# Kernel tuning notes

Measured on AMD Instinct MI355X. Metric: run time of the kernel, lower is better.

The kernel has to match this reference:

```python
import jax, jax.numpy as jnp
import numpy as np

B, T, E, H = 64, 577, 768, 64
GRID_H, GRID_W = 24, 24
NUM_PREFIX = 1
N = GRID_H * GRID_W  # 576 patches
EPS = 1e-5


def setup_inputs() -> dict:
    key = jax.random.key(0)
    ks = jax.random.split(key, 12)
    s = lambda k, shape, fan: jax.random.normal(k, shape, jnp.float32) / np.sqrt(fan)
    return {
        "x": jax.random.normal(ks[0], (B, T, E), jnp.float32),
        "w_q": s(ks[1], (E, H), E),
        "w_k": s(ks[2], (E, H), E),
        "w_v": s(ks[3], (E, H), E),
        "q_gamma": jnp.ones((H,), jnp.float32),
        "q_beta": jnp.zeros((H,), jnp.float32),
        "k_gamma": jnp.ones((H,), jnp.float32),
        "k_beta": jnp.zeros((H,), jnp.float32),
        "w_sigma": s(ks[4], (H, 2), H),
        "b_sigma": jnp.zeros((2,), jnp.float32),
        "w_alpha": s(ks[5], (H, 1), H),
        "b_alpha": jnp.zeros((1,), jnp.float32),
    }


def _layernorm(x, gamma, beta):
    mu = jnp.mean(x, axis=-1, keepdims=True)
    var = jnp.mean(jnp.square(x - mu), axis=-1, keepdims=True)
    return (x - mu) * jax.lax.rsqrt(var + EPS) * gamma + beta


def _grid_sq_dists():
    # coords[i] = (row, col) of patch i; squared coordinate differences [N, N]
    coords = jnp.stack(
        jnp.meshgrid(jnp.arange(GRID_H), jnp.arange(GRID_W), indexing="ij"), axis=-1
    ).reshape(N, 2).astype(jnp.float32)
    diff = coords[:, None, :] - coords[None, :, :]  # [N, N, 2]
    dy2 = jnp.square(diff[..., 0])  # row diff squared
    dx2 = jnp.square(diff[..., 1])  # col diff squared
    return dx2, dy2


def reference(x, w_q, w_k, w_v, q_gamma, q_beta, k_gamma, k_beta,
              w_sigma, b_sigma, w_alpha, b_alpha):
    q = _layernorm(x @ w_q, q_gamma, q_beta)  # [B, T, H]
    k = _layernorm(x @ w_k, k_gamma, k_beta)  # [B, T, H]
    v = x @ w_v                               # [B, T, H]

    sim = jnp.einsum("bqh,bkh->bqk", q, k)    # [B, T, T]

    q_nc = q[:, NUM_PREFIX:, :]               # [B, N, H]
    alpha = jax.nn.softplus(q_nc @ w_alpha + b_alpha)[..., 0]  # [B, N]
    sigma = jax.nn.sigmoid(q_nc @ w_sigma + b_sigma)           # [B, N, 2]
    sx = sigma[..., 0]  # [B, N]
    sy = sigma[..., 1]

    dx2, dy2 = _grid_sq_dists()  # [N, N] each
    # Gaussian decay bias: query-patch p controls sigma; [B, N, N]
    G = jnp.exp(
        -dx2[None] / (2.0 * jnp.square(sx)[:, :, None])
        - dy2[None] / (2.0 * jnp.square(sy)[:, :, None])
    )
    S = alpha[:, :, None] * G

    sim = sim.at[:, NUM_PREFIX:, NUM_PREFIX:].add(S)

    scale = jnp.sqrt(jnp.float32(H))
    attn = jax.nn.softmax(sim / scale, axis=-1)
    return attn @ v  # [B, T, H]
```

## Files before the change

kernel.cpp:

```cpp
#include <hip/hip_runtime.h>
#include <math.h>

#define B_ 64
#define T_ 577
#define E_ 768
#define H_ 64
#define N_ 576
#define GW_ 24

typedef float f32x4 __attribute__((ext_vector_type(4)));
typedef __bf16 bf16x8 __attribute__((ext_vector_type(8)));
typedef __bf16 bf16x4 __attribute__((ext_vector_type(4)));

__device__ inline void split_bf16(float f, __bf16& h, __bf16& l) {
  h = (__bf16)f;
  l = (__bf16)(f - (float)h);
}

__device__ inline float bperm_f(int byte_addr, float x) {
  return __int_as_float(__builtin_amdgcn_ds_bpermute(byte_addr, __float_as_int(x)));
}

#define GLOAD_LDS16(G, L)                                                     \
  __builtin_amdgcn_global_load_lds(                                           \
      (const __attribute__((address_space(1))) void*)(G),                     \
      (__attribute__((address_space(3))) void*)(L), 16, 0, 0)

__global__ __launch_bounds__(256) void prep_w_kernel(
    const float* __restrict__ wq, const float* __restrict__ wk, const float* __restrict__ wv,
    __bf16* __restrict__ wsw2)
{
  int t = blockIdx.x * 256 + threadIdx.x;
  if (t >= 24*192) return;
  int kc = t / 192, n = t - kc*192;
  const float* src = (n < 64) ? wq : ((n < 128) ? wk : wv);
  int nn = n & 63;
  int xb = (n & 3) ^ ((n >> 2) & 3);
  size_t cbase = (size_t)kc * 12288;
  #pragma unroll
  for (int g = 0; g < 4; ++g) {
    __bf16 hb[8], lb[8];
    #pragma unroll
    for (int j = 0; j < 8; ++j) {
      float f = src[(size_t)(kc*32 + g*8 + j)*64 + nn];
      split_bf16(f, hb[j], lb[j]);
    }
    int slot = n*4 + (g ^ xb);
    *(bf16x8*)(wsw2 + cbase + slot*8)        = *(bf16x8*)hb;
    *(bf16x8*)(wsw2 + cbase + 6144 + slot*8) = *(bf16x8*)lb;
  }
}

__global__ __launch_bounds__(256) void qkv_ln_kernel(
    const float* __restrict__ x, const __bf16* __restrict__ wsw2,
    const float* __restrict__ qg, const float* __restrict__ qb,
    const float* __restrict__ kg, const float* __restrict__ kb,
    const float* __restrict__ wsig, const float* __restrict__ bsig,
    const float* __restrict__ walp, const float* __restrict__ balp,
    float* __restrict__ qo, float* __restrict__ ko, float* __restrict__ vo,
    float* __restrict__ alo, float* __restrict__ sxo, float* __restrict__ syo)
{
  __shared__ __align__(16) float smem[64*193 + 256];
  __bf16* A_hi = (__bf16*)smem;
  __bf16* A_lo = A_hi + 2560;
  __bf16* B0   = A_lo + 2560;
  float (*Cs)[193] = (float (*)[193])smem;
  float* mu_q = smem + 64*193;
  float* rs_q = mu_q + 64;
  float* mu_k = rs_q + 64;
  float* rs_k = mu_k + 64;

  const int tid  = threadIdx.x;
  const int lane = tid & 63;
  const int w    = tid >> 6;
  const int quad = lane >> 4;
  const int m    = lane & 15;
  const int rowbase = blockIdx.x << 6;

  f32x4 acc[4][3];
  #pragma unroll
  for (int mt = 0; mt < 4; ++mt)
    #pragma unroll
    for (int nt = 0; nt < 3; ++nt)
      acc[mt][nt] = (f32x4){0.f, 0.f, 0.f, 0.f};

  const int kfrag = quad * 8;
  const int xl    = quad ^ (m & 3) ^ (m >> 2);

  float4 xr0, xr1;
  const int arow0 = tid >> 3,         ak0 = (tid & 7) * 4;
  const int arow1 = (tid + 256) >> 3, ak1 = (tid & 7) * 4;

  auto load_A = [&](int kc) {
    xr0 = *(const float4*)(x + (size_t)(rowbase + arow0)*E_ + kc*32 + ak0);
    xr1 = *(const float4*)(x + (size_t)(rowbase + arow1)*E_ + kc*32 + ak1);
  };
  auto store_A = [&]() {
    __bf16 h0,l0,h1,l1,h2,l2,h3,l3;
    split_bf16(xr0.x,h0,l0); split_bf16(xr0.y,h1,l1);
    split_bf16(xr0.z,h2,l2); split_bf16(xr0.w,h3,l3);
    *(bf16x4*)&A_hi[arow0*40 + ak0] = (bf16x4){h0,h1,h2,h3};
    *(bf16x4*)&A_lo[arow0*40 + ak0] = (bf16x4){l0,l1,l2,l3};
    split_bf16(xr1.x,h0,l0); split_bf16(xr1.y,h1,l1);
    split_bf16(xr1.z,h2,l2); split_bf16(xr1.w,h3,l3);
    *(bf16x4*)&A_hi[arow1*40 + ak1] = (bf16x4){h0,h1,h2,h3};
    *(bf16x4*)&A_lo[arow1*40 + ak1] = (bf16x4){l0,l1,l2,l3};
  };
  auto issue_B = [&](int kc) {
    const __bf16* sbase = wsw2 + (size_t)kc*12288 + (size_t)(w*6)*512 + lane*8;
    __bf16* dbase = B0 + (w*6)*512;
    #pragma unroll
    for (int j = 0; j < 6; ++j)
      GLOAD_LDS16(sbase + j*512, dbase + j*512);
  };

  issue_B(0);
  load_A(0);
  #pragma unroll 1
  for (int kc = 0; kc < 24; ++kc) {
    __syncthreads();
    store_A();
    bf16x8 bh[3], bl[3];
    #pragma unroll
    for (int nt = 0; nt < 3; ++nt) {
      int slotb = (w*48 + nt*16 + m)*4 + xl;
      bh[nt] = *(const bf16x8*)&B0[slotb*8];
      bl[nt] = *(const bf16x8*)&B0[6144 + slotb*8];
    }
    __syncthreads();
    if (kc < 23) {
      issue_B(kc + 1);
      load_A(kc + 1);
    }

    #pragma unroll
    for (int mt = 0; mt < 4; ++mt) {
      bf16x8 ah = *(const bf16x8*)&A_hi[(mt*16 + m)*40 + kfrag];
      bf16x8 al = *(const bf16x8*)&A_lo[(mt*16 + m)*40 + kfrag];
      #pragma unroll
      for (int nt = 0; nt < 3; ++nt) {
        acc[mt][nt] = __builtin_amdgcn_mfma_f32_16x16x32_bf16(ah, bh[nt], acc[mt][nt], 0, 0, 0);
        acc[mt][nt] = __builtin_amdgcn_mfma_f32_16x16x32_bf16(al, bh[nt], acc[mt][nt], 0, 0, 0);
        acc[mt][nt] = __builtin_amdgcn_mfma_f32_16x16x32_bf16(ah, bl[nt], acc[mt][nt], 0, 0, 0);
      }
    }
  }
  __syncthreads();

  #pragma unroll
  for (int mt = 0; mt < 4; ++mt)
    #pragma unroll
    for (int nt = 0; nt < 3; ++nt) {
      int row = mt*16 + quad*4;
      int col = w*48 + nt*16 + m;
      Cs[row + 0][col] = acc[mt][nt].x;
      Cs[row + 1][col] = acc[mt][nt].y;
      Cs[row + 2][col] = acc[mt][nt].z;
      Cs[row + 3][col] = acc[mt][nt].w;
    }
  __syncthreads();

  if (tid < 64) {
    float s = 0.f;
    for (int h = 0; h < 64; ++h) s += Cs[tid][h];
    float mu = s * (1.f/64.f);
    float vs = 0.f;
    for (int h = 0; h < 64; ++h) { float d = Cs[tid][h] - mu; vs += d*d; }
    mu_q[tid] = mu;
    rs_q[tid] = rsqrtf(vs*(1.f/64.f) + 1e-5f);
  } else if (tid < 128) {
    int r = tid - 64;
    float s = 0.f;
    for (int h = 0; h < 64; ++h) s += Cs[r][64+h];
    float mu = s * (1.f/64.f);
    float vs = 0.f;
    for (int h = 0; h < 64; ++h) { float d = Cs[r][64+h] - mu; vs += d*d; }
    mu_k[r] = mu;
    rs_k[r] = rsqrtf(vs*(1.f/64.f) + 1e-5f);
  }
  __syncthreads();

  if (tid >= 192) {
    int r = tid - 192;
    int mrow = rowbase + r;
    int tindex = mrow % T_;
    if (tindex >= 1) {
      int bb = mrow / T_;
      int g = tindex - 1;
      float mu = mu_q[r], rs = rs_q[r];
      float za = 0.f, z0 = 0.f, z1 = 0.f;
      for (int h = 0; h < 64; ++h) {
        float qv = (Cs[r][h] - mu) * rs * qg[h] + qb[h];
        za += qv * walp[h];
        z0 += qv * wsig[2*h];
        z1 += qv * wsig[2*h+1];
      }
      za += balp[0]; z0 += bsig[0]; z1 += bsig[1];
      float al = fmaxf(za, 0.f) + log1pf(__expf(-fabsf(za)));
      float sx = 1.f/(1.f + __expf(-z0));
      float sy = 1.f/(1.f + __expf(-z1));
      alo[bb*N_ + g] = al;
      sxo[bb*N_ + g] = 0.5f/(sx*sx);
      syo[bb*N_ + g] = 0.5f/(sy*sy);
    }
  }
  for (int idx = tid; idx < 64*48; idx += 256) {
    int r = idx / 48, c4 = (idx - (idx/48)*48) * 4;
    size_t row = (size_t)rowbase + r;
    float4 val = make_float4(Cs[r][c4], Cs[r][c4+1], Cs[r][c4+2], Cs[r][c4+3]);
    if (c4 < 64) {
      float mu = mu_q[r], rs = rs_q[r];
      float4 o;
      o.x = (val.x - mu)*rs*qg[c4+0] + qb[c4+0];
      o.y = (val.y - mu)*rs*qg[c4+1] + qb[c4+1];
      o.z = (val.z - mu)*rs*qg[c4+2] + qb[c4+2];
      o.w = (val.w - mu)*rs*qg[c4+3] + qb[c4+3];
      *(float4*)(qo + row*64 + c4) = o;
    } else if (c4 < 128) {
      int h = c4 - 64;
      float mu = mu_k[r], rs = rs_k[r];
      float4 o;
      o.x = (val.x - mu)*rs*kg[h+0] + kb[h+0];
      o.y = (val.y - mu)*rs*kg[h+1] + kb[h+1];
      o.z = (val.z - mu)*rs*kg[h+2] + kb[h+2];
      o.w = (val.w - mu)*rs*kg[h+3] + kb[h+3];
      *(float4*)(ko + row*64 + h) = o;
    } else {
      *(float4*)(vo + row*64 + (c4-128)) = val;
    }
  }
}

__global__ __launch_bounds__(256, 4) void attn_kernel(
    const float* __restrict__ q, const float* __restrict__ k, const float* __restrict__ v,
    const float* __restrict__ ala, const float* __restrict__ sxa, const float* __restrict__ sya,
    float* __restrict__ out)
{
  __shared__ __align__(16) __bf16 sm[4*4608];
  __bf16* KH = sm;            __bf16* KL = sm + 4608;
  __bf16* VH = sm + 2*4608;   __bf16* VL = sm + 3*4608;

  const int tid  = threadIdx.x;
  const int lane = tid & 63;
  const int w    = tid >> 6;
  const int quad = lane >> 4;
  const int m    = lane & 15;

  const int f       = blockIdx.y * 10 + blockIdx.x;
  const int logical = (f & 7) * 80 + (f >> 3);
  const int b       = logical / 10;
  const int qt      = logical - b * 10;

  const float* qbase = q + (size_t)b * T_ * H_;
  const float* kbase = k + (size_t)b * T_ * H_;
  const float* vbase = v + (size_t)b * T_ * H_;

  const int  row    = qt*64 + w*16 + m;
  const int  rowc   = row < T_ ? row : T_ - 1;
  const bool qvalid = row < T_;
  const bool qhas   = (row >= 1) && qvalid;
  float al = 0.f, isx = 0.f, isy = 0.f, qr = 0.f, qc = 0.f;
  {
    int g = qhas ? row - 1 : 0;
    if (qhas) {
      al  = ala[b*N_ + g] * 0.125f;
      isx = sxa[b*N_ + g];
      isy = sya[b*N_ + g];
      int gr = g / GW_;
      qr = (float)gr;
      qc = (float)(g - gr*GW_);
    }
  }

  bf16x8 qh[2], ql[2];
  #pragma unroll
  for (int ks = 0; ks < 2; ++ks) {
    float4 f0 = *(const float4*)(qbase + (size_t)rowc*H_ + ks*32 + quad*8);
    float4 f1 = *(const float4*)(qbase + (size_t)rowc*H_ + ks*32 + quad*8 + 4);
    float fv[8] = {f0.x, f0.y, f0.z, f0.w, f1.x, f1.y, f1.z, f1.w};
    #pragma unroll
    for (int j = 0; j < 8; ++j) {
      float s = fv[j] * 0.125f;
      __bf16 h, l;
      split_bf16(s, h, l);
      qh[ks][j] = h;
      ql[ks][j] = l;
    }
  }

  float mo = -INFINITY, lsum = 0.f;
  f32x4 acc[4];
  #pragma unroll
  for (int nt = 0; nt < 4; ++nt) acc[nt] = (f32x4){0.f, 0.f, 0.f, 0.f};

  const int  addrA = ((2*(quad & 1))*16 + m) * 4;
  const int  addrB = addrA + 64;
  const bool hiNT  = quad >= 2;

  float4 kreg[4];
  float  vreg[16];
  const int d0 = tid & 15, k0 = (tid >> 4) * 4;

  auto load_kv = [&](int kt) {
    #pragma unroll
    for (int i = 0; i < 4; ++i) {
      int s = tid + 256*i;
      int key = s >> 4, c4 = (s & 15)*4;
      int kgl = kt*64 + key;
      int kcl = kgl < T_ ? kgl : T_ - 1;
      kreg[i] = *(const float4*)(kbase + (size_t)kcl*H_ + c4);
    }
    #pragma unroll
    for (int di = 0; di < 4; ++di)
      #pragma unroll
      for (int ki = 0; ki < 4; ++ki) {
        int kgl = kt*64 + k0 + ki;
        int kcl = kgl < T_ ? kgl : T_ - 1;
        vreg[di*4+ki] = vbase[(size_t)kcl*H_ + d0 + 16*di];
      }
  };
  auto store_kv = [&]() {
    #pragma unroll
    for (int i = 0; i < 4; ++i) {
      int s = tid + 256*i;
      int key = s >> 4, c4 = (s & 15)*4;
      __bf16 h0,l0,h1,l1,h2,l2,h3,l3;
      split_bf16(kreg[i].x,h0,l0); split_bf16(kreg[i].y,h1,l1);
      split_bf16(kreg[i].z,h2,l2); split_bf16(kreg[i].w,h3,l3);
      *(bf16x4*)&KH[key*72 + c4] = (bf16x4){h0,h1,h2,h3};
      *(bf16x4*)&KL[key*72 + c4] = (bf16x4){l0,l1,l2,l3};
    }
    #pragma unroll
    for (int di = 0; di < 4; ++di) {
      int dim = d0 + 16*di;
      __bf16 h0,l0,h1,l1,h2,l2,h3,l3;
      split_bf16(vreg[di*4+0],h0,l0); split_bf16(vreg[di*4+1],h1,l1);
      split_bf16(vreg[di*4+2],h2,l2); split_bf16(vreg[di*4+3],h3,l3);
      *(bf16x4*)&VH[dim*72 + k0] = (bf16x4){h0,h1,h2,h3};
      *(bf16x4*)&VL[dim*72 + k0] = (bf16x4){l0,l1,l2,l3};
    }
  };

  load_kv(0);
  #pragma unroll 1
  for (int kt = 0; kt < 10; ++kt) {
    __syncthreads();
    store_kv();
    __syncthreads();
    if (kt < 9) load_kv(kt + 1);

    float s_[4][4];
    #pragma unroll
    for (int nt = 0; nt < 4; ++nt) {
      f32x4 sac = (f32x4){0.f, 0.f, 0.f, 0.f};
      #pragma unroll
      for (int ks = 0; ks < 2; ++ks) {
        const int ko_ = ks*32 + quad*8;
        bf16x8 kh = *(const bf16x8*)&KH[(nt*16 + m)*72 + ko_];
        bf16x8 kl = *(const bf16x8*)&KL[(nt*16 + m)*72 + ko_];
        sac = __builtin_amdgcn_mfma_f32_16x16x32_bf16(kh, qh[ks], sac, 0, 0, 0);
        sac = __builtin_amdgcn_mfma_f32_16x16x32_bf16(kl, qh[ks], sac, 0, 0, 0);
        sac = __builtin_amdgcn_mfma_f32_16x16x32_bf16(kh, ql[ks], sac, 0, 0, 0);
      }
      s_[nt][0] = sac.x; s_[nt][1] = sac.y; s_[nt][2] = sac.z; s_[nt][3] = sac.w;
    }

    #pragma unroll
    for (int nt = 0; nt < 4; ++nt) {
      #pragma unroll
      for (int reg = 0; reg < 4; ++reg) {
        int key = kt*64 + nt*16 + quad*4 + reg;
        float sval = s_[nt][reg];
        float kgf = (float)(key - 1);
        float krf = floorf(kgf * (1.0f/24.0f));
        float kcf = kgf - 24.f*krf;
        float dx = qc - kcf, dy = qr - krf;
        float bias = al * __expf(-(dx*dx*isx + dy*dy*isy));
        bool khas = (key >= 1) && (key < T_);
        sval += (khas && qhas) ? bias : 0.f;
        s_[nt][reg] = (key < T_) ? sval : -1e30f;
      }
    }

    float mx = s_[0][0];
    #pragma unroll
    for (int nt = 0; nt < 4; ++nt)
      #pragma unroll
      for (int reg = 0; reg < 4; ++reg)
        mx = fmaxf(mx, s_[nt][reg]);
    mx = fmaxf(mx, __shfl_xor(mx, 16, 64));
    mx = fmaxf(mx, __shfl_xor(mx, 32, 64));
    float mn = fmaxf(mo, mx);
    float sc = __expf(mo - mn);
    float lt = 0.f;
    #pragma unroll
    for (int nt = 0; nt < 4; ++nt)
      #pragma unroll
      for (int reg = 0; reg < 4; ++reg) {
        float p = __expf(s_[nt][reg] - mn);
        s_[nt][reg] = p;
        lt += p;
      }
    lt += __shfl_xor(lt, 16, 64);
    lt += __shfl_xor(lt, 32, 64);
    lsum = lsum*sc + lt;
    mo = mn;
    #pragma unroll
    for (int nt = 0; nt < 4; ++nt) {
      acc[nt].x *= sc; acc[nt].y *= sc; acc[nt].z *= sc; acc[nt].w *= sc;
    }

    bf16x8 fh[2], fl[2];
    #pragma unroll
    for (int ks = 0; ks < 2; ++ks) {
      #pragma unroll
      for (int reg = 0; reg < 4; ++reg) {
        float xa0 = bperm_f(addrA, s_[2*ks+0][reg]);
        float xa1 = bperm_f(addrA, s_[2*ks+1][reg]);
        float xb0 = bperm_f(addrB, s_[2*ks+0][reg]);
        float xb1 = bperm_f(addrB, s_[2*ks+1][reg]);
        float va = hiNT ? xa1 : xa0;
        float vb = hiNT ? xb1 : xb0;
        __bf16 h, l;
        split_bf16(va, h, l); fh[ks][reg]   = h; fl[ks][reg]   = l;
        split_bf16(vb, h, l); fh[ks][4+reg] = h; fl[ks][4+reg] = l;
      }
    }

    #pragma unroll
    for (int nt = 0; nt < 4; ++nt) {
      f32x4 c = acc[nt];
      #pragma unroll
      for (int ks = 0; ks < 2; ++ks) {
        const int ko_ = ks*32 + quad*8;
        bf16x8 vh = *(const bf16x8*)&VH[(nt*16 + m)*72 + ko_];
        bf16x8 vl = *(const bf16x8*)&VL[(nt*16 + m)*72 + ko_];
        c = __builtin_amdgcn_mfma_f32_16x16x32_bf16(vh, fh[ks], c, 0, 0, 0);
        c = __builtin_amdgcn_mfma_f32_16x16x32_bf16(vl, fh[ks], c, 0, 0, 0);
        c = __builtin_amdgcn_mfma_f32_16x16x32_bf16(vh, fl[ks], c, 0, 0, 0);
      }
      acc[nt] = c;
    }
  }

  if (qvalid) {
    float inv = 1.f / lsum;
    #pragma unroll
    for (int nt = 0; nt < 4; ++nt) {
      float4 o;
      o.x = acc[nt].x * inv;
      o.y = acc[nt].y * inv;
      o.z = acc[nt].z * inv;
      o.w = acc[nt].w * inv;
      *(float4*)(out + ((size_t)b*T_ + row)*H_ + nt*16 + quad*4) = o;
    }
  }
}

extern "C" void kernel_launch(void* const* d_in, const int* in_sizes, int n_in,
                              void* d_out, int out_size, void* d_ws, size_t ws_size,
                              hipStream_t stream) {
  const float* x      = (const float*)d_in[0];
  const float* wq     = (const float*)d_in[1];
  const float* wk     = (const float*)d_in[2];
  const float* wv     = (const float*)d_in[3];
  const float* qg     = (const float*)d_in[4];
  const float* qb     = (const float*)d_in[5];
  const float* kg     = (const float*)d_in[6];
  const float* kb     = (const float*)d_in[7];
  const float* wsig   = (const float*)d_in[8];
  const float* bsig   = (const float*)d_in[9];
  const float* walp   = (const float*)d_in[10];
  const float* balp   = (const float*)d_in[11];
  float* out = (float*)d_out;

  float* ws  = (float*)d_ws;
  const size_t nrow = (size_t)B_ * T_;
  float* qo  = ws;
  float* ko  = qo + nrow*H_;
  float* vo  = ko + nrow*H_;
  float* alo = vo + nrow*H_;
  float* sxo = alo + (size_t)B_*N_;
  float* syo = sxo + (size_t)B_*N_;
  __bf16* wsw2 = (__bf16*)(syo + (size_t)B_*N_);

  hipLaunchKernelGGL(prep_w_kernel, dim3(18), dim3(256), 0, stream,
                     wq, wk, wv, wsw2);
  hipLaunchKernelGGL(qkv_ln_kernel, dim3(577), dim3(256), 0, stream,
                     x, wsw2, qg, qb, kg, kb, wsig, bsig, walp, balp,
                     qo, ko, vo, alo, sxo, syo);
  hipLaunchKernelGGL(attn_kernel, dim3(10, B_), dim3(256), 0, stream,
                     qo, ko, vo, alo, sxo, syo, out);
}
```

Baseline: 287.7 us.

## Double-buffer A tile in LDS and cut QKV GEMM loop to one barrier

The QKV projection GEMM now keeps two LDS buffers for the split hi/lo bf16 A tile. The next tile is written to the spare buffer while the current one feeds the MFMAs, and the global prefetch of x runs two iterations ahead. Each wave's B prefetch now touches only the LDS region that wave reads, hi and lo interleaved. Together this removes one of the two __syncthreads per k-step. In exchange it adds register pressure, more LDS use, and relies on the end-of-loop barrier (and its vmcnt wait) to make the async B loads visible in time.

```diff
diff --git a/kernel.cpp b/kernel.cpp
--- a/kernel.cpp
+++ b/kernel.cpp
@@ -61,9 +61,11 @@
     float* __restrict__ alo, float* __restrict__ sxo, float* __restrict__ syo)
 {
   __shared__ __align__(16) float smem[64*193 + 256];
-  __bf16* A_hi = (__bf16*)smem;
-  __bf16* A_lo = A_hi + 2560;
-  __bf16* B0   = A_lo + 2560;
+  __bf16* A_hi0 = (__bf16*)smem;
+  __bf16* A_lo0 = A_hi0 + 2560;
+  __bf16* A_hi1 = A_lo0 + 2560;
+  __bf16* A_lo1 = A_hi1 + 2560;
+  __bf16* B0    = A_lo1 + 2560;
   float (*Cs)[193] = (float (*)[193])smem;
   float* mu_q = smem + 64*193;
   float* rs_q = mu_q + 64;
@@ -95,31 +97,40 @@
     xr0 = *(const float4*)(x + (size_t)(rowbase + arow0)*E_ + kc*32 + ak0);
     xr1 = *(const float4*)(x + (size_t)(rowbase + arow1)*E_ + kc*32 + ak1);
   };
-  auto store_A = [&]() {
+  auto store_A_to = [&](__bf16* AH, __bf16* AL) {
     __bf16 h0,l0,h1,l1,h2,l2,h3,l3;
     split_bf16(xr0.x,h0,l0); split_bf16(xr0.y,h1,l1);
     split_bf16(xr0.z,h2,l2); split_bf16(xr0.w,h3,l3);
-    *(bf16x4*)&A_hi[arow0*40 + ak0] = (bf16x4){h0,h1,h2,h3};
-    *(bf16x4*)&A_lo[arow0*40 + ak0] = (bf16x4){l0,l1,l2,l3};
+    *(bf16x4*)&AH[arow0*40 + ak0] = (bf16x4){h0,h1,h2,h3};
+    *(bf16x4*)&AL[arow0*40 + ak0] = (bf16x4){l0,l1,l2,l3};
     split_bf16(xr1.x,h0,l0); split_bf16(xr1.y,h1,l1);
     split_bf16(xr1.z,h2,l2); split_bf16(xr1.w,h3,l3);
-    *(bf16x4*)&A_hi[arow1*40 + ak1] = (bf16x4){h0,h1,h2,h3};
-    *(bf16x4*)&A_lo[arow1*40 + ak1] = (bf16x4){l0,l1,l2,l3};
+    *(bf16x4*)&AH[arow1*40 + ak1] = (bf16x4){h0,h1,h2,h3};
+    *(bf16x4*)&AL[arow1*40 + ak1] = (bf16x4){l0,l1,l2,l3};
   };
   auto issue_B = [&](int kc) {
-    const __bf16* sbase = wsw2 + (size_t)kc*12288 + (size_t)(w*6)*512 + lane*8;
-    __bf16* dbase = B0 + (w*6)*512;
-    #pragma unroll
-    for (int j = 0; j < 6; ++j)
-      GLOAD_LDS16(sbase + j*512, dbase + j*512);
+    const size_t roff = (size_t)w * 1536;
+    const __bf16* s_hi = wsw2 + (size_t)kc*12288 + roff + lane*8;
+    const __bf16* s_lo = s_hi + 6144;
+    __bf16* d_hi = B0 + roff;
+    __bf16* d_lo = d_hi + 6144;
+    #pragma unroll
+    for (int j = 0; j < 3; ++j) {
+      GLOAD_LDS16(s_hi + j*512, d_hi + j*512);
+      GLOAD_LDS16(s_lo + j*512, d_lo + j*512);
+    }
   };
 
   issue_B(0);
   load_A(0);
+  store_A_to(A_hi0, A_lo0);
+  load_A(1);
+  __syncthreads();
+
+  __bf16 *cA_hi = A_hi0, *cA_lo = A_lo0, *nA_hi = A_hi1, *nA_lo = A_lo1;
+
   #pragma unroll 1
   for (int kc = 0; kc < 24; ++kc) {
-    __syncthreads();
-    store_A();
     bf16x8 bh[3], bl[3];
     #pragma unroll
     for (int nt = 0; nt < 3; ++nt) {
@@ -127,16 +138,16 @@
       bh[nt] = *(const bf16x8*)&B0[slotb*8];
       bl[nt] = *(const bf16x8*)&B0[6144 + slotb*8];
     }
-    __syncthreads();
-    if (kc < 23) {
-      issue_B(kc + 1);
-      load_A(kc + 1);
-    }
+    if (kc < 23) store_A_to(nA_hi, nA_lo);
+    asm volatile("s_waitcnt lgkmcnt(0)" ::: "memory");
+    __builtin_amdgcn_sched_barrier(0);
+    if (kc < 23) issue_B(kc + 1);
+    if (kc < 22) load_A(kc + 2);
 
     #pragma unroll
     for (int mt = 0; mt < 4; ++mt) {
-      bf16x8 ah = *(const bf16x8*)&A_hi[(mt*16 + m)*40 + kfrag];
-      bf16x8 al = *(const bf16x8*)&A_lo[(mt*16 + m)*40 + kfrag];
+      bf16x8 ah = *(const bf16x8*)&cA_hi[(mt*16 + m)*40 + kfrag];
+      bf16x8 al = *(const bf16x8*)&cA_lo[(mt*16 + m)*40 + kfrag];
       #pragma unroll
       for (int nt = 0; nt < 3; ++nt) {
         acc[mt][nt] = __builtin_amdgcn_mfma_f32_16x16x32_bf16(ah, bh[nt], acc[mt][nt], 0, 0, 0);
@@ -144,8 +155,11 @@
         acc[mt][nt] = __builtin_amdgcn_mfma_f32_16x16x32_bf16(ah, bl[nt], acc[mt][nt], 0, 0, 0);
       }
     }
-  }
-  __syncthreads();
+    __syncthreads();
+    __bf16* t;
+    t = cA_hi; cA_hi = nA_hi; nA_hi = t;
+    t = cA_lo; cA_lo = nA_lo; nA_lo = t;
+  }
 
   #pragma unroll
   for (int mt = 0; mt < 4; ++mt)
```

Measured after the change: 288.5 us. Within noise of the previous version (+0.3%).
